# Kernel optimization log

Measured on AMD Instinct MI355X. Metric: run time of the kernel, lower is better.

Reference implementation:

```python
import jax, jax.numpy as jnp
import numpy as np

N = 40000
E = 640000
D_IN = 128
D_OUT = 128
K = 3
LAMBDA_MAX = 2.0
LN_EPS = 1e-5


def setup_inputs() -> dict:
    key = jax.random.key(0)
    k1, k2, k3, k4, k5 = jax.random.split(key, 5)
    x = jax.random.normal(k1, (N, D_IN), dtype=jnp.float32)
    edge_index = jax.random.randint(k2, (2, E), 0, N, dtype=jnp.int64)
    edge_weight = jax.random.uniform(k3, (E,), dtype=jnp.float32)
    # Chebyshev weights: one [D_IN, D_OUT] matrix per hop k, plus shared bias
    W = jax.random.normal(k4, (K, D_IN, D_OUT), dtype=jnp.float32) / np.sqrt(D_IN)
    bias = jnp.zeros((D_OUT,), dtype=jnp.float32)
    gamma = jnp.ones((D_OUT,), dtype=jnp.float32)
    beta = jnp.zeros((D_OUT,), dtype=jnp.float32)
    return {"x": x, "edge_weight": edge_weight, "W": W, "bias": bias,
            "gamma": gamma, "beta": beta, "edge_index": edge_index}


def reference(x, edge_weight, W, bias, gamma, beta, edge_index):
    row, col = edge_index[0], edge_index[1]

    # Symmetric normalization of the graph Laplacian (PyG ChebConv, norm='sym')
    deg = jax.ops.segment_sum(edge_weight, row, num_segments=N)
    dinv = jnp.where(deg > 0, jax.lax.rsqrt(deg), 0.0)
    # scaled Laplacian L_hat = (2/lambda_max) * (I - A_norm) - I
    # off-diagonal entries: -(2/lambda_max) * a_norm ; diagonal: 2/lambda_max - 1
    scale = 2.0 / LAMBDA_MAX
    norm = -scale * dinv[row] * edge_weight * dinv[col]  # [E]
    diag = scale - 1.0  # == 0 for lambda_max = 2

    def prop(h):  # L_hat @ h via gather / scale / scatter-add
        msg = norm[:, None] * h[col]                      # [E, D]
        return jax.ops.segment_sum(msg, row, num_segments=N) + diag * h

    # Chebyshev recursion: T0 = x, T1 = L_hat x, Tk = 2 L_hat T_{k-1} - T_{k-2}
    Tx0 = x
    out = Tx0 @ W[0]
    Tx1 = prop(x)
    out = out + Tx1 @ W[1]
    for k in range(2, K):
        Tx2 = 2.0 * prop(Tx1) - Tx0
        out = out + Tx2 @ W[k]
        Tx0, Tx1 = Tx1, Tx2
    out = out + bias

    # LayerNorm over channels + ReLU
    mean = jnp.mean(out, axis=-1, keepdims=True)
    var = jnp.var(out, axis=-1, keepdims=True)
    out = (out - mean) * jax.lax.rsqrt(var + LN_EPS) * gamma + beta
    return jax.nn.relu(out)
```

## Files before the change

kernel.cpp:

```cpp
#include <hip/hip_runtime.h>

#define NN 40000
#define EE 640000
#define DD 128
#define CAP 96

typedef __attribute__((ext_vector_type(8))) __bf16 bf16x8;
typedef __attribute__((ext_vector_type(4))) float f32x4;

static __device__ __forceinline__ unsigned short bfs(float f) {
    __bf16 h = (__bf16)f;
    return __builtin_bit_cast(unsigned short, h);
}
static __device__ __forceinline__ float blo(unsigned int v) {
    return __builtin_bit_cast(float, v << 16);
}
static __device__ __forceinline__ float bhi(unsigned int v) {
    return __builtin_bit_cast(float, v & 0xffff0000u);
}

__global__ __launch_bounds__(256) void k_pre(const int* __restrict__ ei,
                                             const float* __restrict__ ew,
                                             const float* __restrict__ x,
                                             const float* __restrict__ W,
                                             unsigned int* __restrict__ degcnt,
                                             int2* __restrict__ pair,
                                             unsigned short* __restrict__ xb,
                                             unsigned short* __restrict__ Wt) {
    int b = blockIdx.x;
    int tid = threadIdx.x;
    if (b < 2500) {
        int e = b * 256 + tid;
        int r = ei[e];
        int c = ei[EE + e];
        float w = ew[e];
        unsigned int q = __float2uint_rn(w * 65536.0f);
        unsigned int old = atomicAdd(degcnt + r, (1u << 24) | q);
        int rk = (int)(old >> 24);
        if (rk < CAP)
            pair[(size_t)r * CAP + rk] = make_int2(c, __float_as_int(w));
    } else if (b < 3125) {
        int base = (b - 2500) * 2048 + tid;
        #pragma unroll
        for (int it = 0; it < 8; it++) {
            int i = base + it * 256;
            float4 v = ((const float4*)x)[i];
            ushort4 p;
            p.x = bfs(v.x); p.y = bfs(v.y); p.z = bfs(v.z); p.w = bfs(v.w);
            ((ushort4*)xb)[i] = p;
        }
    } else {
        int t = (b - 3125) * 256 + tid;
        int n = t / 384;
        int c = t - n * 384;
        Wt[t] = bfs(W[(size_t)c * 128 + n]);
    }
}

__global__ __launch_bounds__(256) void k_dinv(const unsigned int* __restrict__ degcnt,
                                              float* __restrict__ dinv) {
    int i = blockIdx.x * 256 + threadIdx.x;
    if (i < NN) {
        unsigned int lo = degcnt[i] & 0x00ffffffu;
        dinv[i] = lo > 0 ? rsqrtf((float)lo * (1.0f / 65536.0f)) : 0.0f;
    }
}

__global__ __launch_bounds__(256) void k_prop(const unsigned int* __restrict__ degcnt,
                                              const int2* __restrict__ pair,
                                              const unsigned short* __restrict__ hb,
                                              const float* __restrict__ dinv,
                                              const unsigned short* __restrict__ subb,
                                              float alpha, float betac,
                                              unsigned short* __restrict__ outb) {
    int grp = (blockIdx.x * 256 + threadIdx.x) >> 4;
    int q = threadIdx.x & 15;

    int cnt = (int)(degcnt[grp] >> 24);
    if (cnt > CAP) cnt = CAP;
    float dr = dinv[grp];

    int s = grp * CAP, t = s + cnt;
    float a0 = 0.f, a1 = 0.f, a2 = 0.f, a3 = 0.f, a4 = 0.f, a5 = 0.f, a6 = 0.f, a7 = 0.f;

    int e = s;
    int2 p0, p1, p2, p3;
    bool have = (e + 4 <= t);
    if (have) { p0 = pair[e]; p1 = pair[e + 1]; p2 = pair[e + 2]; p3 = pair[e + 3]; }
    while (have) {
        uint4 h0 = *(const uint4*)(hb + (size_t)p0.x * DD + q * 8);
        uint4 h1 = *(const uint4*)(hb + (size_t)p1.x * DD + q * 8);
        uint4 h2 = *(const uint4*)(hb + (size_t)p2.x * DD + q * 8);
        uint4 h3 = *(const uint4*)(hb + (size_t)p3.x * DD + q * 8);
        float n0 = __int_as_float(p0.y) * dinv[p0.x];
        float n1 = __int_as_float(p1.y) * dinv[p1.x];
        float n2 = __int_as_float(p2.y) * dinv[p2.x];
        float n3 = __int_as_float(p3.y) * dinv[p3.x];
        int en = e + 4;
        have = (en + 4 <= t);
        if (have) { p0 = pair[en]; p1 = pair[en + 1]; p2 = pair[en + 2]; p3 = pair[en + 3]; }
        e = en;
        a0 = fmaf(n0, blo(h0.x), a0); a1 = fmaf(n0, bhi(h0.x), a1);
        a2 = fmaf(n0, blo(h0.y), a2); a3 = fmaf(n0, bhi(h0.y), a3);
        a4 = fmaf(n0, blo(h0.z), a4); a5 = fmaf(n0, bhi(h0.z), a5);
        a6 = fmaf(n0, blo(h0.w), a6); a7 = fmaf(n0, bhi(h0.w), a7);
        a0 = fmaf(n1, blo(h1.x), a0); a1 = fmaf(n1, bhi(h1.x), a1);
        a2 = fmaf(n1, blo(h1.y), a2); a3 = fmaf(n1, bhi(h1.y), a3);
        a4 = fmaf(n1, blo(h1.z), a4); a5 = fmaf(n1, bhi(h1.z), a5);
        a6 = fmaf(n1, blo(h1.w), a6); a7 = fmaf(n1, bhi(h1.w), a7);
        a0 = fmaf(n2, blo(h2.x), a0); a1 = fmaf(n2, bhi(h2.x), a1);
        a2 = fmaf(n2, blo(h2.y), a2); a3 = fmaf(n2, bhi(h2.y), a3);
        a4 = fmaf(n2, blo(h2.z), a4); a5 = fmaf(n2, bhi(h2.z), a5);
        a6 = fmaf(n2, blo(h2.w), a6); a7 = fmaf(n2, bhi(h2.w), a7);
        a0 = fmaf(n3, blo(h3.x), a0); a1 = fmaf(n3, bhi(h3.x), a1);
        a2 = fmaf(n3, blo(h3.y), a2); a3 = fmaf(n3, bhi(h3.y), a3);
        a4 = fmaf(n3, blo(h3.z), a4); a5 = fmaf(n3, bhi(h3.z), a5);
        a6 = fmaf(n3, blo(h3.w), a6); a7 = fmaf(n3, bhi(h3.w), a7);
    }
    if (e < t) {
        int i1 = (e + 1 < t) ? e + 1 : t - 1;
        int i2 = (e + 2 < t) ? e + 2 : t - 1;
        float m1 = (e + 1 < t) ? 1.f : 0.f;
        float m2 = (e + 2 < t) ? 1.f : 0.f;
        int2 q0 = pair[e];
        int2 q1 = pair[i1];
        int2 q2 = pair[i2];
        uint4 h0 = *(const uint4*)(hb + (size_t)q0.x * DD + q * 8);
        uint4 h1 = *(const uint4*)(hb + (size_t)q1.x * DD + q * 8);
        uint4 h2 = *(const uint4*)(hb + (size_t)q2.x * DD + q * 8);
        float n0 = __int_as_float(q0.y) * dinv[q0.x];
        float n1 = m1 * __int_as_float(q1.y) * dinv[q1.x];
        float n2 = m2 * __int_as_float(q2.y) * dinv[q2.x];
        a0 = fmaf(n0, blo(h0.x), a0); a1 = fmaf(n0, bhi(h0.x), a1);
        a2 = fmaf(n0, blo(h0.y), a2); a3 = fmaf(n0, bhi(h0.y), a3);
        a4 = fmaf(n0, blo(h0.z), a4); a5 = fmaf(n0, bhi(h0.z), a5);
        a6 = fmaf(n0, blo(h0.w), a6); a7 = fmaf(n0, bhi(h0.w), a7);
        a0 = fmaf(n1, blo(h1.x), a0); a1 = fmaf(n1, bhi(h1.x), a1);
        a2 = fmaf(n1, blo(h1.y), a2); a3 = fmaf(n1, bhi(h1.y), a3);
        a4 = fmaf(n1, blo(h1.z), a4); a5 = fmaf(n1, bhi(h1.z), a5);
        a6 = fmaf(n1, blo(h1.w), a6); a7 = fmaf(n1, bhi(h1.w), a7);
        a0 = fmaf(n2, blo(h2.x), a0); a1 = fmaf(n2, bhi(h2.x), a1);
        a2 = fmaf(n2, blo(h2.y), a2); a3 = fmaf(n2, bhi(h2.y), a3);
        a4 = fmaf(n2, blo(h2.z), a4); a5 = fmaf(n2, bhi(h2.z), a5);
        a6 = fmaf(n2, blo(h2.w), a6); a7 = fmaf(n2, bhi(h2.w), a7);
    }

    float scale = -alpha * dr;
    if (subb != nullptr) {
        const unsigned short* sp = subb + (size_t)grp * DD + q * 8;
        uint4 sv = *(const uint4*)sp;
        a0 = fmaf(scale, a0, betac * blo(sv.x));
        a1 = fmaf(scale, a1, betac * bhi(sv.x));
        a2 = fmaf(scale, a2, betac * blo(sv.y));
        a3 = fmaf(scale, a3, betac * bhi(sv.y));
        a4 = fmaf(scale, a4, betac * blo(sv.z));
        a5 = fmaf(scale, a5, betac * bhi(sv.z));
        a6 = fmaf(scale, a6, betac * blo(sv.w));
        a7 = fmaf(scale, a7, betac * bhi(sv.w));
    } else {
        a0 *= scale; a1 *= scale; a2 *= scale; a3 *= scale;
        a4 *= scale; a5 *= scale; a6 *= scale; a7 *= scale;
    }
    ushort4 o0, o1;
    o0.x = bfs(a0); o0.y = bfs(a1); o0.z = bfs(a2); o0.w = bfs(a3);
    o1.x = bfs(a4); o1.y = bfs(a5); o1.z = bfs(a6); o1.w = bfs(a7);
    unsigned short* op = outb + (size_t)grp * DD + q * 8;
    *(ushort4*)(op) = o0;
    *(ushort4*)(op + 4) = o1;
}

__global__ __launch_bounds__(320) void k_gemm_mfma_ln(
        const unsigned short* __restrict__ xb, const unsigned short* __restrict__ t1b,
        const unsigned short* __restrict__ t2b, const unsigned short* __restrict__ Wt,
        const float* __restrict__ bias, const float* __restrict__ gamma,
        const float* __restrict__ beta, float* __restrict__ out) {
    int tid = threadIdx.x;
    int lane = tid & 63;
    int wv = tid >> 6;
    int quad = lane >> 4;
    int l15 = lane & 15;
    int rowq = blockIdx.x * 160 + wv * 32;

    int r0 = rowq + l15;
    int r1 = rowq + 16 + l15;

    float bias_l[8], gamma_l[8], beta_l[8];
    #pragma unroll
    for (int nt = 0; nt < 8; nt++) {
        int cc = nt * 16 + l15;
        bias_l[nt] = bias[cc];
        gamma_l[nt] = gamma[cc];
        beta_l[nt] = beta[cc];
    }

    f32x4 acc[2][8];
    #pragma unroll
    for (int mt = 0; mt < 2; mt++)
        #pragma unroll
        for (int nt = 0; nt < 8; nt++)
            acc[mt][nt] = (f32x4){0.f, 0.f, 0.f, 0.f};

    #pragma unroll
    for (int c = 0; c < 12; c++) {
        const unsigned short* src = (c < 4) ? xb : ((c < 8) ? t1b : t2b);
        int kk = (c & 3) * 32 + quad * 8;
        bf16x8 a0 = *(const bf16x8*)(src + (size_t)r0 * DD + kk);
        bf16x8 a1 = *(const bf16x8*)(src + (size_t)r1 * DD + kk);
        #pragma unroll
        for (int nt = 0; nt < 8; nt++) {
            bf16x8 b = *(const bf16x8*)(Wt + (size_t)(nt * 16 + l15) * 384 + c * 32 + quad * 8);
            acc[0][nt] = __builtin_amdgcn_mfma_f32_16x16x32_bf16(a0, b, acc[0][nt], 0, 0, 0);
            acc[1][nt] = __builtin_amdgcn_mfma_f32_16x16x32_bf16(a1, b, acc[1][nt], 0, 0, 0);
        }
    }

    #pragma unroll
    for (int mt = 0; mt < 2; mt++) {
        #pragma unroll
        for (int reg = 0; reg < 4; reg++) {
            float v[8];
            float s = 0.f, sq = 0.f;
            #pragma unroll
            for (int nt = 0; nt < 8; nt++) {
                v[nt] = acc[mt][nt][reg] + bias_l[nt];
                s += v[nt];
                sq += v[nt] * v[nt];
            }
            #pragma unroll
            for (int m = 1; m <= 8; m <<= 1) {
                s  += __shfl_xor(s, m, 64);
                sq += __shfl_xor(sq, m, 64);
            }
            float mean = s * (1.0f / 128.0f);
            float var = sq * (1.0f / 128.0f) - mean * mean;
            float inv = rsqrtf(var + 1e-5f);
            int grow = rowq + mt * 16 + quad * 4 + reg;
            #pragma unroll
            for (int nt = 0; nt < 8; nt++) {
                float o = fmaxf((v[nt] - mean) * inv * gamma_l[nt] + beta_l[nt], 0.0f);
                out[(size_t)grow * DD + nt * 16 + l15] = o;
            }
        }
    }
}

extern "C" void kernel_launch(void* const* d_in, const int* in_sizes, int n_in,
                              void* d_out, int out_size, void* d_ws, size_t ws_size,
                              hipStream_t stream) {
    const float* x     = (const float*)d_in[0];
    const float* ew    = (const float*)d_in[1];
    const float* W     = (const float*)d_in[2];
    const float* bias  = (const float*)d_in[3];
    const float* gamma = (const float*)d_in[4];
    const float* beta  = (const float*)d_in[5];
    const int*   ei    = (const int*)d_in[6];
    float* out = (float*)d_out;

    char* ws = (char*)d_ws;
    size_t o = 0;
    auto alloc = [&](size_t bytes) { void* p = ws + o; o += (bytes + 255) & ~(size_t)255; return p; };
    unsigned int* degcnt = (unsigned int*)alloc((size_t)NN * 4);
    float* dinv  = (float*)alloc((size_t)NN * 4);
    int2*  pair  = (int2*) alloc((size_t)NN * CAP * 8);
    unsigned short* xb  = (unsigned short*)alloc((size_t)NN * DD * 2);
    unsigned short* t1b = (unsigned short*)alloc((size_t)NN * DD * 2);
    unsigned short* t2b = (unsigned short*)alloc((size_t)NN * DD * 2);
    unsigned short* Wt  = (unsigned short*)alloc((size_t)384 * 128 * 2);

    hipMemsetAsync(degcnt, 0, (size_t)NN * 4, stream);

    k_pre<<<3317, 256, 0, stream>>>(ei, ew, x, W, degcnt, pair, xb, Wt);
    k_dinv<<<(NN + 255) / 256, 256, 0, stream>>>(degcnt, dinv);

    k_prop<<<NN / 16, 256, 0, stream>>>(degcnt, pair, xb, dinv, nullptr, 1.0f, 0.0f, t1b);
    k_prop<<<NN / 16, 256, 0, stream>>>(degcnt, pair, t1b, dinv, xb, 2.0f, -1.0f, t2b);

    k_gemm_mfma_ln<<<250, 320, 0, stream>>>(xb, t1b, t2b, Wt, bias, gamma, beta, out);
}
```

Before: 193.3 us.

## Build row adjacency with a bucketed counting sort instead of global atomics

Edge-list construction now runs in several passes. Each block first builds a per-block histogram of edges over 128-row buckets. A single block then prefix-scans those histograms, and a scatter pass writes edge records into contiguous bucket ranges. A final pass uses shared-memory 64-bit atomics to compute per-row counts, weighted degrees and the padded pair lists, and it also produces dinv, so the memset and the separate dinv kernel are gone. The aim is to replace contended, randomly scattered global atomics and pair writes with local atomics and bucket-local writes. The cost is extra launches, a serial single-block scan, and roughly 20 MB of extra intermediate traffic.

```diff
diff --git a/kernel.cpp b/kernel.cpp
--- a/kernel.cpp
+++ b/kernel.cpp
@@ -4,9 +4,13 @@
 #define EE 640000
 #define DD 128
 #define CAP 96
+#define NBE 128
+#define EPB 5000
+#define NBK 320
 
 typedef __attribute__((ext_vector_type(8))) __bf16 bf16x8;
 typedef __attribute__((ext_vector_type(4))) float f32x4;
+typedef unsigned long long ull;
 
 static __device__ __forceinline__ unsigned short bfs(float f) {
     __bf16 h = (__bf16)f;
@@ -19,28 +23,31 @@
     return __builtin_bit_cast(float, v & 0xffff0000u);
 }
 
-__global__ __launch_bounds__(256) void k_pre(const int* __restrict__ ei,
-                                             const float* __restrict__ ew,
-                                             const float* __restrict__ x,
-                                             const float* __restrict__ W,
-                                             unsigned int* __restrict__ degcnt,
-                                             int2* __restrict__ pair,
-                                             unsigned short* __restrict__ xb,
-                                             unsigned short* __restrict__ Wt) {
+__global__ __launch_bounds__(256) void kA(const int* __restrict__ ei,
+                                          const float* __restrict__ x,
+                                          const float* __restrict__ W,
+                                          int* __restrict__ ghist,
+                                          unsigned short* __restrict__ xb,
+                                          unsigned short* __restrict__ Wt) {
     int b = blockIdx.x;
     int tid = threadIdx.x;
-    if (b < 2500) {
-        int e = b * 256 + tid;
-        int r = ei[e];
-        int c = ei[EE + e];
-        float w = ew[e];
-        unsigned int q = __float2uint_rn(w * 65536.0f);
-        unsigned int old = atomicAdd(degcnt + r, (1u << 24) | q);
-        int rk = (int)(old >> 24);
-        if (rk < CAP)
-            pair[(size_t)r * CAP + rk] = make_int2(c, __float_as_int(w));
-    } else if (b < 3125) {
-        int base = (b - 2500) * 2048 + tid;
+    if (b < NBE) {
+        __shared__ int h[NBK];
+        for (int k = tid; k < NBK; k += 256) h[k] = 0;
+        __syncthreads();
+        int e0 = b * EPB;
+        #pragma unroll
+        for (int it = 0; it < 20; it++) {
+            int e = e0 + it * 256 + tid;
+            if (e < e0 + EPB) {
+                int r = ei[e];
+                atomicAdd(&h[r >> 7], 1);
+            }
+        }
+        __syncthreads();
+        for (int k = tid; k < NBK; k += 256) ghist[b * NBK + k] = h[k];
+    } else if (b < 753) {
+        int base = (b - NBE) * 2048 + tid;
         #pragma unroll
         for (int it = 0; it < 8; it++) {
             int i = base + it * 256;
@@ -50,19 +57,91 @@
             ((ushort4*)xb)[i] = p;
         }
     } else {
-        int t = (b - 3125) * 256 + tid;
+        int t = (b - 753) * 256 + tid;
         int n = t / 384;
         int c = t - n * 384;
         Wt[t] = bfs(W[(size_t)c * 128 + n]);
     }
 }
 
-__global__ __launch_bounds__(256) void k_dinv(const unsigned int* __restrict__ degcnt,
-                                              float* __restrict__ dinv) {
-    int i = blockIdx.x * 256 + threadIdx.x;
-    if (i < NN) {
-        unsigned int lo = degcnt[i] & 0x00ffffffu;
-        dinv[i] = lo > 0 ? rsqrtf((float)lo * (1.0f / 65536.0f)) : 0.0f;
+__global__ __launch_bounds__(NBK) void kB(const int* __restrict__ ghist,
+                                          int* __restrict__ gbase,
+                                          int* __restrict__ bstart) {
+    __shared__ int sc[2][NBK];
+    int k = threadIdx.x;
+    int s = 0;
+    for (int b = 0; b < NBE; b++) {
+        int t = ghist[b * NBK + k];
+        gbase[b * NBK + k] = s;
+        s += t;
+    }
+    sc[0][k] = s;
+    __syncthreads();
+    int src = 0;
+    #pragma unroll
+    for (int off = 1; off < NBK; off <<= 1) {
+        sc[1 - src][k] = sc[src][k] + ((k >= off) ? sc[src][k - off] : 0);
+        __syncthreads();
+        src ^= 1;
+    }
+    int excl = sc[src][k] - s;
+    bstart[k] = excl;
+    for (int b = 0; b < NBE; b++)
+        gbase[b * NBK + k] += excl;
+}
+
+__global__ __launch_bounds__(256) void kC(const int* __restrict__ ei,
+                                          const float* __restrict__ ew,
+                                          const int* __restrict__ gbase,
+                                          int4* __restrict__ barr) {
+    __shared__ int rank[NBK];
+    int b = blockIdx.x;
+    int tid = threadIdx.x;
+    for (int k = tid; k < NBK; k += 256) rank[k] = gbase[b * NBK + k];
+    __syncthreads();
+    int e0 = b * EPB;
+    #pragma unroll
+    for (int it = 0; it < 20; it++) {
+        int e = e0 + it * 256 + tid;
+        if (e < e0 + EPB) {
+            int r = ei[e];
+            int c = ei[EE + e];
+            float w = ew[e];
+            int slot = atomicAdd(&rank[r >> 7], 1);
+            barr[slot] = make_int4(r, c, __float_as_int(w), 0);
+        }
+    }
+}
+
+__global__ __launch_bounds__(256) void kD(const int4* __restrict__ barr,
+                                          const int* __restrict__ bstart,
+                                          int2* __restrict__ pair,
+                                          unsigned int* __restrict__ degcnt,
+                                          float* __restrict__ dinv) {
+    __shared__ ull cd[128];
+    int k = blockIdx.x;
+    int tid = threadIdx.x;
+    if (tid < 128) cd[tid] = 0;
+    __syncthreads();
+    int rs = bstart[k], re = bstart[k + 1];
+    for (int i = rs + tid; i < re; i += 256) {
+        int4 rec = barr[i];
+        unsigned int q = __float2uint_rn(__int_as_float(rec.z) * 16777216.0f);
+        ull old = atomicAdd(&cd[rec.x & 127], (1ULL << 32) | (ull)q);
+        int rk = (int)(old >> 32);
+        if (rk < CAP)
+            pair[(size_t)rec.x * CAP + rk] = make_int2(rec.y, rec.z);
+    }
+    __syncthreads();
+    if (tid < 128) {
+        int row = (k << 7) + tid;
+        if (row < NN) {
+            ull v = cd[tid];
+            unsigned int cnt = (unsigned int)(v >> 32);
+            unsigned int lo = (unsigned int)v;
+            degcnt[row] = cnt << 24;
+            dinv[row] = lo ? rsqrtf((float)lo * (1.0f / 16777216.0f)) : 0.0f;
+        }
     }
 }
 
@@ -259,6 +338,10 @@
     char* ws = (char*)d_ws;
     size_t o = 0;
     auto alloc = [&](size_t bytes) { void* p = ws + o; o += (bytes + 255) & ~(size_t)255; return p; };
+    int*  ghist  = (int*) alloc((size_t)NBE * NBK * 4);
+    int*  gbase  = (int*) alloc((size_t)NBE * NBK * 4);
+    int*  bstart = (int*) alloc((size_t)(NBK + 1) * 4);
+    int4* barr   = (int4*)alloc((size_t)EE * 16);
     unsigned int* degcnt = (unsigned int*)alloc((size_t)NN * 4);
     float* dinv  = (float*)alloc((size_t)NN * 4);
     int2*  pair  = (int2*) alloc((size_t)NN * CAP * 8);
@@ -267,10 +350,10 @@
     unsigned short* t2b = (unsigned short*)alloc((size_t)NN * DD * 2);
     unsigned short* Wt  = (unsigned short*)alloc((size_t)384 * 128 * 2);
 
-    hipMemsetAsync(degcnt, 0, (size_t)NN * 4, stream);
-
-    k_pre<<<3317, 256, 0, stream>>>(ei, ew, x, W, degcnt, pair, xb, Wt);
-    k_dinv<<<(NN + 255) / 256, 256, 0, stream>>>(degcnt, dinv);
+    kA<<<945, 256, 0, stream>>>(ei, x, W, ghist, xb, Wt);
+    kB<<<1, NBK, 0, stream>>>(ghist, gbase, bstart);
+    kC<<<NBE, 256, 0, stream>>>(ei, ew, gbase, barr);
+    kD<<<313, 256, 0, stream>>>(barr, bstart, pair, degcnt, dinv);
 
     k_prop<<<NN / 16, 256, 0, stream>>>(degcnt, pair, xb, dinv, nullptr, 1.0f, 0.0f, t1b);
     k_prop<<<NN / 16, 256, 0, stream>>>(degcnt, pair, t1b, dinv, xb, 2.0f, -1.0f, t2b);
```

Result: slower. 204.4 us (+5.7%).
